# Performance work log

Hardware: AMD Instinct MI355X
Metric: run time of the kernel (lower is better)

Reference implementation:

```python
import jax, jax.numpy as jnp
import numpy as np

L, B, S, D, H, V = 6, 4, 1024, 1024, 16, 32000
HD = D // H          # head_size = 64
F = 4 * D            # ffn hidden
EPS = 1e-5           # nn.LayerNorm default


def setup_inputs() -> dict:
    key = jax.random.key(0)
    ks = jax.random.split(key, 12)
    s = 0.02
    p = {
        "tokens": jax.random.randint(ks[0], (B, S), 0, V, dtype=jnp.int32),
        "tok_emb": s * jax.random.normal(ks[1], (V, D), jnp.float32),
        "pos_emb": s * jax.random.normal(ks[2], (S, D), jnp.float32),
        # stacked per-layer params (leading dim L)
        "Wq": s * jax.random.normal(ks[3], (L, D, D), jnp.float32),
        "Wk": s * jax.random.normal(ks[4], (L, D, D), jnp.float32),
        "Wv": s * jax.random.normal(ks[5], (L, D, D), jnp.float32),
        "Wp": s * jax.random.normal(ks[6], (L, D, D), jnp.float32),
        "ln1_s": jnp.ones((L, D), jnp.float32),
        "ln1_b": jnp.zeros((L, D), jnp.float32),
        "W1": s * jax.random.normal(ks[7], (L, D, F), jnp.float32),
        "b1": jnp.zeros((L, F), jnp.float32),
        "W2": s * jax.random.normal(ks[8], (L, F, D), jnp.float32),
        "b2": jnp.zeros((L, D), jnp.float32),
        "ln2_s": jnp.ones((L, D), jnp.float32),
        "ln2_b": jnp.zeros((L, D), jnp.float32),
        "lnf_s": jnp.ones((D,), jnp.float32),
        "lnf_b": jnp.zeros((D,), jnp.float32),
        "Wh": s * jax.random.normal(ks[9], (D, V), jnp.float32),
        "bh": jnp.zeros((V,), jnp.float32),
    }
    return p


def _ln(x, scale, bias):
    m = x.mean(-1, keepdims=True)
    v = ((x - m) ** 2).mean(-1, keepdims=True)
    return (x - m) * jax.lax.rsqrt(v + EPS) * scale + bias


def reference(tokens, tok_emb, pos_emb, Wq, Wk, Wv, Wp, ln1_s, ln1_b,
              W1, b1, W2, b2, ln2_s, ln2_b, lnf_s, lnf_b, Wh, bh):
    x = tok_emb[tokens] + pos_emb[None, :, :]            # [B,S,D]
    mask = jnp.tril(jnp.ones((S, S), dtype=bool))
    inv_sqrt_hd = HD ** -0.5

    def layer(x, p):
        wq, wk, wv, wp, l1s, l1b, w1, b1_, w2, b2_, l2s, l2b = p
        q = jnp.einsum('bsd,dhk->bhsk', x, wq.reshape(D, H, HD))
        k = jnp.einsum('bsd,dhk->bhsk', x, wk.reshape(D, H, HD))
        v = jnp.einsum('bsd,dhk->bhsk', x, wv.reshape(D, H, HD))
        scores = jnp.einsum('bhsk,bhtk->bhst', q, k)     # [B,H,S,S]
        # original: masked_fill(-inf) THEN * head_size**-0.5 (same math: -inf stays -inf)
        scores = jnp.where(mask, scores * inv_sqrt_hd, -jnp.inf)
        attn = jax.nn.softmax(scores, axis=-1)
        o = jnp.einsum('bhst,bhtk->bhsk', attn, v)
        o = o.transpose(0, 2, 1, 3).reshape(B, S, D) @ wp
        a = x + _ln(o, l1s, l1b)                          # residual + ln1 (as in source)
        f = jax.nn.relu(a @ w1 + b1_) @ w2 + b2_
        return x + _ln(f, l2s, l2b), None                 # residual from block INPUT (as in source)

    x, _ = jax.lax.scan(layer, x,
                        (Wq, Wk, Wv, Wp, ln1_s, ln1_b, W1, b1, W2, b2, ln2_s, ln2_b))
    return _ln(x, lnf_s, lnf_b) @ Wh + bh                 # [B,S,V]
```

## Files before the change

### kernel.cpp

```cpp
#include <hip/hip_runtime.h>

#define DEV __device__ __forceinline__

typedef __attribute__((ext_vector_type(4))) float f32x4;
typedef __attribute__((ext_vector_type(8))) short short8_t;

constexpr int LNUM = 6;
constexpr int BB = 4;
constexpr int SS = 1024;
constexpr int DD = 1024;
constexpr int HH = 16;
constexpr int HDD = 64;
constexpr int FF = 4096;
constexpr int VV = 32000;
constexpr int MROWS = BB * SS;

DEV short f2bf(float f) {
  union { float f; unsigned u; } x; x.f = f;
  unsigned r = x.u + 0x7fffu + ((x.u >> 16) & 1u);
  return (short)(r >> 16);
}

#define BAR() do { __builtin_amdgcn_sched_barrier(0); \
  __builtin_amdgcn_s_barrier(); \
  __builtin_amdgcn_sched_barrier(0); } while (0)

__global__ __launch_bounds__(256) void k_embed(
    const int* __restrict__ tok, const float* __restrict__ te,
    const float* __restrict__ pe, float* __restrict__ xf,
    short* __restrict__ xb) {
  int i = blockIdx.x * 256 + threadIdx.x;
  int bs = i >> 8, d4 = i & 255;
  int t = tok[bs];
  float4 a = ((const float4*)(te + (size_t)t * DD))[d4];
  float4 b = ((const float4*)(pe + (size_t)(bs & (SS - 1)) * DD))[d4];
  float4 r; r.x = a.x + b.x; r.y = a.y + b.y; r.z = a.z + b.z; r.w = a.w + b.w;
  ((float4*)xf)[i] = r;
  short4 o; o.x = f2bf(r.x); o.y = f2bf(r.y); o.z = f2bf(r.z); o.w = f2bf(r.w);
  ((short4*)xb)[i] = o;
}

__global__ __launch_bounds__(256) void k_tcvt(
    const float* __restrict__ in, short* __restrict__ out, int K, int N,
    long long ostride) {
  __shared__ float tile[32][33];
  const float* ip = in + (size_t)blockIdx.z * K * N;
  short* op = out + (size_t)blockIdx.z * ostride;
  int bn = blockIdx.x * 32, bk = blockIdx.y * 32;
  int tx = threadIdx.x, ty = threadIdx.y;
  #pragma unroll
  for (int r = 0; r < 32; r += 8)
    tile[ty + r][tx] = ip[(size_t)(bk + ty + r) * N + bn + tx];
  __syncthreads();
  #pragma unroll
  for (int r = 0; r < 32; r += 8)
    op[(size_t)(bn + ty + r) * K + bk + tx] = f2bf(tile[tx][ty + r]);
}

DEV void gload16(const short* g, short* l) {
  __builtin_amdgcn_global_load_lds(
      (const __attribute__((address_space(1))) void*)g,
      (__attribute__((address_space(3))) void*)l, 16, 0, 0);
}

template<int MODE>
__global__ __launch_bounds__(512, 2) void k_gemm256(
    const short* __restrict__ A, const short* __restrict__ Bt,
    const float* __restrict__ bias, void* __restrict__ Cp,
    int M, int N, int K, int lda, int ldb) {
  extern __shared__ short lds[];
  const int tid = threadIdx.x;
  const int nbx = gridDim.x;
  const int nwg = nbx << 4;
  const int hid = blockIdx.y * nbx + blockIdx.x;
  const int cpx = nwg >> 3;
  const int lid = (hid & 7) * cpx + (hid >> 3);
  const int bx = lid >> 4, by = lid & 15;
  const int n0 = bx * 256, m0 = by * 256;

  const int lane = tid & 63;
  const int wid = tid >> 6;
  const int wm = wid >> 2, wn = wid & 3;
  const int l16 = lane & 15, kg = lane >> 4;
  const int xorv = (l16 & 7) << 4;
  const int cs[2] = { ((kg << 4) ^ xorv) >> 1,
                      ((64 | (kg << 4)) ^ xorv) >> 1 };
  const int rr = tid >> 3;
  const int sce = ((((tid & 7) << 4) ^ ((rr & 7) << 4)) >> 1);
  const int ldst = (tid & ~63) * 8;

  const int NT = K >> 6;

  auto stageA = [&](int t2, int c2) {
    const int k0 = t2 << 6;
    const int base = c2 * 32768;
    #pragma unroll
    for (int h = 0; h < 2; h++)
      #pragma unroll
      for (int li = 0; li < 2; li++)
        gload16(A + (size_t)(m0 + h * 128 + li * 64 + rr) * lda + k0 + sce,
                &lds[base + h * 8192 + li * 4096 + ldst]);
  };
  auto stageB = [&](int t2, int c2) {
    const int k0 = t2 << 6;
    const int base = c2 * 32768 + 16384;
    #pragma unroll
    for (int h = 0; h < 2; h++)
      #pragma unroll
      for (int li = 0; li < 2; li++)
        gload16(Bt + (size_t)(n0 + h * 128 + li * 64 + rr) * ldb + k0 + sce,
                &lds[base + h * 8192 + li * 4096 + ldst]);
  };

  f32x4 acc[8][4];
  #pragma unroll
  for (int mi = 0; mi < 8; mi++)
    #pragma unroll
    for (int ni = 0; ni < 4; ni++)
      #pragma unroll
      for (int j = 0; j < 4; j++) acc[mi][ni][j] = 0.f;

  stageA(0, 0); stageB(0, 0);
  stageA(1, 1); stageB(1, 1);
  asm volatile("s_waitcnt vmcnt(8)" ::: "memory");
  BAR();

  for (int t = 0; t < NT; t++) {
    const int c = t & 1;
    const int ao = c * 32768 + wm * 8192;
    const int bo = c * 32768 + 16384 + (wn >> 1) * 8192 + (wn & 1) * 4096;
    short8_t a[4][2], b0[2][2], b1[2][2];

    #pragma unroll
    for (int mi = 0; mi < 4; mi++)
      #pragma unroll
      for (int kk = 0; kk < 2; kk++)
        a[mi][kk] = *(const short8_t*)&lds[ao + (mi * 16 + l16) * 64 + cs[kk]];
    #pragma unroll
    for (int ni = 0; ni < 2; ni++)
      #pragma unroll
      for (int kk = 0; kk < 2; kk++)
        b0[ni][kk] = *(const short8_t*)&lds[bo + (ni * 16 + l16) * 64 + cs[kk]];
    BAR();
    __builtin_amdgcn_s_setprio(1);
    #pragma unroll
    for (int mi = 0; mi < 4; mi++)
      #pragma unroll
      for (int ni = 0; ni < 2; ni++)
        #pragma unroll
        for (int kk = 0; kk < 2; kk++)
          acc[mi][ni] = __builtin_amdgcn_mfma_f32_16x16x32_bf16(
              a[mi][kk], b0[ni][kk], acc[mi][ni], 0, 0, 0);
    __builtin_amdgcn_s_setprio(0);
    BAR();

    #pragma unroll
    for (int ni = 0; ni < 2; ni++)
      #pragma unroll
      for (int kk = 0; kk < 2; kk++)
        b1[ni][kk] = *(const short8_t*)&lds[bo + ((ni + 2) * 16 + l16) * 64 + cs[kk]];
    BAR();
    __builtin_amdgcn_s_setprio(1);
    #pragma unroll
    for (int mi = 0; mi < 4; mi++)
      #pragma unroll
      for (int ni = 0; ni < 2; ni++)
        #pragma unroll
        for (int kk = 0; kk < 2; kk++)
          acc[mi][ni + 2] = __builtin_amdgcn_mfma_f32_16x16x32_bf16(
              a[mi][kk], b1[ni][kk], acc[mi][ni + 2], 0, 0, 0);
    __builtin_amdgcn_s_setprio(0);
    BAR();

    #pragma unroll
    for (int mi = 0; mi < 4; mi++)
      #pragma unroll
      for (int kk = 0; kk < 2; kk++)
        a[mi][kk] = *(const short8_t*)&lds[ao + ((mi + 4) * 16 + l16) * 64 + cs[kk]];
    if (t + 2 < NT) stageB(t + 2, c);
    BAR();
    __builtin_amdgcn_s_setprio(1);
    #pragma unroll
    for (int mi = 0; mi < 4; mi++)
      #pragma unroll
      for (int ni = 0; ni < 2; ni++)
        #pragma unroll
        for (int kk = 0; kk < 2; kk++)
          acc[mi + 4][ni + 2] = __builtin_amdgcn_mfma_f32_16x16x32_bf16(
              a[mi][kk], b1[ni][kk], acc[mi + 4][ni + 2], 0, 0, 0);
    __builtin_amdgcn_s_setprio(0);
    BAR();

    if (t + 2 < NT) stageA(t + 2, c);
    BAR();
    __builtin_amdgcn_s_setprio(1);
    #pragma unroll
    for (int mi = 0; mi < 4; mi++)
      #pragma unroll
      for (int ni = 0; ni < 2; ni++)
        #pragma unroll
        for (int kk = 0; kk < 2; kk++)
          acc[mi + 4][ni] = __builtin_amdgcn_mfma_f32_16x16x32_bf16(
              a[mi][kk], b0[ni][kk], acc[mi + 4][ni], 0, 0, 0);
    __builtin_amdgcn_s_setprio(0);
    if (t + 2 < NT) asm volatile("s_waitcnt vmcnt(8)" ::: "memory");
    else            asm volatile("s_waitcnt vmcnt(0)" ::: "memory");
    BAR();
  }

  #pragma unroll
  for (int mi = 0; mi < 8; mi++) {
    #pragma unroll
    for (int ni = 0; ni < 4; ni++) {
      #pragma unroll
      for (int j = 0; j < 4; j++) {
        const int r = m0 + wm * 128 + mi * 16 + kg * 4 + j;
        const int c = n0 + wn * 64 + ni * 16 + l16;
        const float v = acc[mi][ni][j];
        if (MODE == 5) {
          ((float*)Cp)[(size_t)r * N + c] = v;
        } else if (MODE == 6) {
          ((short*)Cp)[(size_t)r * N + c] = f2bf(fmaxf(v + bias[c], 0.f));
        } else if (MODE == 7) {
          ((float*)Cp)[(size_t)r * N + c] = v + bias[c];
        } else if (MODE == 8) {
          int kind = c >> 10, cc = c & 1023;
          int b = r >> 10, s = r & 1023, h = cc >> 6, hd = cc & 63;
          size_t off;
          if (kind < 2)
            off = (size_t)kind * MROWS * DD +
                  (((size_t)(b * HH + h) << 10) + s) * HDD + hd;
          else
            off = (size_t)2 * MROWS * DD +
                  (((size_t)(b * HH + h) * HDD + hd) << 10) + s;
          ((short*)Cp)[off] = f2bf(v);
        }
      }
    }
  }
}

#define RDSWZ(arr, r, cb) \
  (*(const short8_t*)&arr[((r) << 6) + ((((cb) ^ (((r) & 7) << 4))) >> 1)])
#define RDSWZ7(arr, r, cb) \
  (*(const short8_t*)&arr[((r) << 7) + ((((cb) ^ (((r) & 7) << 4))) >> 1)])

__global__ __launch_bounds__(256, 2) void k_attn(
    const short* __restrict__ Qg, const short* __restrict__ Kgl,
    const short* __restrict__ Vt, short* __restrict__ Og) {
  extern __shared__ short sm[];
  short* lQ = sm;
  short* lK = sm + 8192;
  short* lV = sm + 16384;
  short* lP = sm + 24576;
  const int tid = threadIdx.x;
  const int qb = blockIdx.x, z = blockIdx.y;
  const int q0 = qb << 7;
  const short* Qp = Qg + ((size_t)z << 16);
  const short* Kp = Kgl + ((size_t)z << 16);
  const short* Vp = Vt + ((size_t)z << 16);
  const int bidx = z >> 4, h = z & 15;
  const int lane = tid & 63, w = tid >> 6;
  const int l16 = lane & 15, kg = lane >> 4;
  const int sr = tid >> 3;
  const int scb = ((((tid & 7) << 4) ^ ((sr & 7) << 4)) >> 1);
  const int vr = tid >> 4;
  const int vcb = ((((tid & 15) << 4) ^ ((vr & 7) << 4)) >> 1);
  const int ldst = (tid & ~63) << 3;

  #pragma unroll
  for (int i = 0; i < 4; i++)
    gload16(Qp + ((size_t)(q0 + i * 32 + sr) << 6) + scb, &lQ[i * 2048 + ldst]);

  f32x4 acc_o[2][4];
  float m_r[2][4], l_r[2][4];
  #pragma unroll
  for (int mi = 0; mi < 2; mi++)
    #pragma unroll
    for (int j = 0; j < 4; j++) {
      m_r[mi][j] = -3e38f; l_r[mi][j] = 0.f;
      #pragma unroll
      for (int n2 = 0; n2 < 4; n2++) acc_o[mi][n2][j] = 0.f;
    }

  const int nkt = qb + 1;
  for (int kt = 0; kt < nkt; kt++) {
    const int k0 = kt << 7;
    #pragma unroll
    for (int i = 0; i < 4; i++)
      gload16(Kp + ((size_t)(k0 + i * 32 + sr) << 6) + scb, &lK[i * 2048 + ldst]);
    #pragma unroll
    for (int i = 0; i < 4; i++)
      gload16(Vp + ((size_t)(i * 16 + vr) << 10) + k0 + vcb, &lV[i * 2048 + ldst]);
    __syncthreads();

    f32x4 s[2][8];
    #pragma unroll
    for (int mi = 0; mi < 2; mi++)
      #pragma unroll
      for (int nf = 0; nf < 8; nf++)
        #pragma unroll
        for (int j = 0; j < 4; j++) s[mi][nf][j] = 0.f;
    #pragma unroll
    for (int kk = 0; kk < 2; kk++) {
      short8_t aq[2];
      #pragma unroll
      for (int mi = 0; mi < 2; mi++)
        aq[mi] = RDSWZ(lQ, w * 32 + mi * 16 + l16, kk * 64 + kg * 16);
      #pragma unroll
      for (int nf = 0; nf < 8; nf++) {
        short8_t bk = RDSWZ(lK, nf * 16 + l16, kk * 64 + kg * 16);
        #pragma unroll
        for (int mi = 0; mi < 2; mi++)
          s[mi][nf] = __builtin_amdgcn_mfma_f32_16x16x32_bf16(
              aq[mi], bk, s[mi][nf], 0, 0, 0);
      }
    }

    const bool diag = (kt == qb);
    #pragma unroll
    for (int mi = 0; mi < 2; mi++) {
      #pragma unroll
      for (int j = 0; j < 4; j++) {
        const int ql = w * 32 + mi * 16 + kg * 4 + j;
        const int q = q0 + ql;
        float sv[8]; float tm = -3e38f;
        #pragma unroll
        for (int nf = 0; nf < 8; nf++) {
          int kv = k0 + nf * 16 + l16;
          sv[nf] = (!diag || kv <= q) ? s[mi][nf][j] * 0.125f : -3e38f;
          tm = fmaxf(tm, sv[nf]);
        }
        #pragma unroll
        for (int o = 1; o < 16; o <<= 1) tm = fmaxf(tm, __shfl_xor(tm, o));
        const float mn = fmaxf(m_r[mi][j], tm);
        const float scale = __expf(m_r[mi][j] - mn);
        float e[8]; float ts = 0.f;
        #pragma unroll
        for (int nf = 0; nf < 8; nf++) { e[nf] = __expf(sv[nf] - mn); ts += e[nf]; }
        #pragma unroll
        for (int o = 1; o < 16; o <<= 1) ts += __shfl_xor(ts, o);
        l_r[mi][j] = l_r[mi][j] * scale + ts;
        m_r[mi][j] = mn;
        #pragma unroll
        for (int n2 = 0; n2 < 4; n2++) acc_o[mi][n2][j] *= scale;
        #pragma unroll
        for (int nf = 0; nf < 8; nf++)
          lP[(ql << 7) + ((nf * 16 + l16) ^ ((ql & 7) << 3))] = f2bf(e[nf]);
      }
    }

    #pragma unroll
    for (int kc = 0; kc < 4; kc++) {
      short8_t pa[2];
      #pragma unroll
      for (int mi = 0; mi < 2; mi++) {
        const int pr = w * 32 + mi * 16 + l16;
        pa[mi] = *(const short8_t*)
            &lP[(pr << 7) + ((kc * 32 + kg * 8) ^ ((pr & 7) << 3))];
      }
      #pragma unroll
      for (int n2 = 0; n2 < 4; n2++) {
        short8_t vb = RDSWZ7(lV, n2 * 16 + l16, kc * 64 + kg * 16);
        #pragma unroll
        for (int mi = 0; mi < 2; mi++)
          acc_o[mi][n2] = __builtin_amdgcn_mfma_f32_16x16x32_bf16(
              pa[mi], vb, acc_o[mi][n2], 0, 0, 0);
      }
    }
    __syncthreads();
  }

  #pragma unroll
  for (int mi = 0; mi < 2; mi++) {
    #pragma unroll
    for (int j = 0; j < 4; j++) {
      const int q = q0 + w * 32 + mi * 16 + kg * 4 + j;
      const float inv = 1.f / l_r[mi][j];
      #pragma unroll
      for (int n2 = 0; n2 < 4; n2++) {
        const int col = h * HDD + n2 * 16 + l16;
        Og[(((size_t)bidx << 10) + q) * DD + col] = f2bf(acc_o[mi][n2][j] * inv);
      }
    }
  }
}

template<int ADD_RES, int WRITE_F32>
__global__ __launch_bounds__(256) void k_ln(
    const float* __restrict__ src, const float* __restrict__ res,
    const float* __restrict__ g, const float* __restrict__ b,
    float* __restrict__ of, short* __restrict__ ob) {
  const int row = blockIdx.x;
  const int tid = threadIdx.x;
  float4 v = ((const float4*)(src + ((size_t)row << 10)))[tid];
  float s1 = v.x + v.y + v.z + v.w;
  float s2 = v.x * v.x + v.y * v.y + v.z * v.z + v.w * v.w;
  #pragma unroll
  for (int o = 32; o; o >>= 1) { s1 += __shfl_xor(s1, o); s2 += __shfl_xor(s2, o); }
  __shared__ float sh1[4], sh2[4];
  if ((tid & 63) == 0) { sh1[tid >> 6] = s1; sh2[tid >> 6] = s2; }
  __syncthreads();
  s1 = sh1[0] + sh1[1] + sh1[2] + sh1[3];
  s2 = sh2[0] + sh2[1] + sh2[2] + sh2[3];
  const float mean = s1 * (1.f / 1024.f);
  const float var  = s2 * (1.f / 1024.f) - mean * mean;
  const float rs = rsqrtf(var + 1e-5f);
  float4 gg = ((const float4*)g)[tid];
  float4 bb = ((const float4*)b)[tid];
  float4 o4;
  o4.x = (v.x - mean) * rs * gg.x + bb.x;
  o4.y = (v.y - mean) * rs * gg.y + bb.y;
  o4.z = (v.z - mean) * rs * gg.z + bb.z;
  o4.w = (v.w - mean) * rs * gg.w + bb.w;
  if (ADD_RES) {
    float4 rr = ((const float4*)(res + ((size_t)row << 10)))[tid];
    o4.x += rr.x; o4.y += rr.y; o4.z += rr.z; o4.w += rr.w;
  }
  if (WRITE_F32) ((float4*)(of + ((size_t)row << 10)))[tid] = o4;
  short4 s4; s4.x = f2bf(o4.x); s4.y = f2bf(o4.y);
  s4.z = f2bf(o4.z); s4.w = f2bf(o4.w);
  ((short4*)ob)[((size_t)row << 8) + tid] = s4;
}

extern "C" void kernel_launch(void* const* d_in, const int* in_sizes, int n_in,
                              void* d_out, int out_size, void* d_ws, size_t ws_size,
                              hipStream_t stream) {
  (void)in_sizes; (void)n_in; (void)out_size; (void)ws_size;
  const int*   tokens  = (const int*)d_in[0];
  const float* tok_emb = (const float*)d_in[1];
  const float* pos_emb = (const float*)d_in[2];
  const float* Wq = (const float*)d_in[3];
  const float* Wk = (const float*)d_in[4];
  const float* Wv = (const float*)d_in[5];
  const float* Wp = (const float*)d_in[6];
  const float* ln1s = (const float*)d_in[7];
  const float* ln1b = (const float*)d_in[8];
  const float* W1 = (const float*)d_in[9];
  const float* b1 = (const float*)d_in[10];
  const float* W2 = (const float*)d_in[11];
  const float* b2 = (const float*)d_in[12];
  const float* ln2s = (const float*)d_in[13];
  const float* ln2b = (const float*)d_in[14];
  const float* lnfs = (const float*)d_in[15];
  const float* lnfb = (const float*)d_in[16];
  const float* Wh = (const float*)d_in[17];
  const float* bh = (const float*)d_in[18];
  float* out = (float*)d_out;

  hipFuncSetAttribute((const void*)k_gemm256<5>,
      hipFuncAttributeMaxDynamicSharedMemorySize, 131072);
  hipFuncSetAttribute((const void*)k_gemm256<6>,
      hipFuncAttributeMaxDynamicSharedMemorySize, 131072);
  hipFuncSetAttribute((const void*)k_gemm256<7>,
      hipFuncAttributeMaxDynamicSharedMemorySize, 131072);
  hipFuncSetAttribute((const void*)k_gemm256<8>,
      hipFuncAttributeMaxDynamicSharedMemorySize, 131072);
  hipFuncSetAttribute((const void*)k_attn,
      hipFuncAttributeMaxDynamicSharedMemorySize, 81920);

  char* p = (char*)d_ws;
  auto alloc = [&](size_t elems, size_t esz) -> char* {
    char* r = p; p += (elems * esz + 255) & ~(size_t)255; return r;
  };
  short* WqkvT = (short*)alloc((size_t)LNUM * 3 * DD * DD, 2);
  short* WpT = (short*)alloc((size_t)LNUM * DD * DD, 2);
  short* W1T = (short*)alloc((size_t)LNUM * DD * FF, 2);
  short* W2T = (short*)alloc((size_t)LNUM * DD * FF, 2);
  short* WhT = (short*)alloc((size_t)DD * VV, 2);
  float* xf   = (float*)alloc((size_t)MROWS * DD, 4);
  float* ff   = (float*)alloc((size_t)MROWS * DD, 4);
  short* xb   = (short*)alloc((size_t)MROWS * DD, 2);
  short* ab   = (short*)alloc((size_t)MROWS * DD, 2);
  short* qkvb = (short*)alloc((size_t)3 * MROWS * DD, 2);
  short* obuf = (short*)alloc((size_t)MROWS * DD, 2);
  short* hb   = (short*)alloc((size_t)MROWS * FF, 2);
  short* xfb  = (short*)alloc((size_t)MROWS * DD, 2);
  short* qb   = qkvb;
  short* kb   = qkvb + (size_t)MROWS * DD;
  short* vtb  = qkvb + (size_t)2 * MROWS * DD;

  dim3 blk(256);
  dim3 t8(32, 8);
  const long long DD2 = (long long)DD * DD;
  k_tcvt<<<dim3(DD / 32, DD / 32, LNUM), t8, 0, stream>>>(Wq, WqkvT,          DD, DD, 3 * DD2);
  k_tcvt<<<dim3(DD / 32, DD / 32, LNUM), t8, 0, stream>>>(Wk, WqkvT + DD2,    DD, DD, 3 * DD2);
  k_tcvt<<<dim3(DD / 32, DD / 32, LNUM), t8, 0, stream>>>(Wv, WqkvT + 2*DD2,  DD, DD, 3 * DD2);
  k_tcvt<<<dim3(DD / 32, DD / 32, LNUM), t8, 0, stream>>>(Wp, WpT, DD, DD, DD2);
  k_tcvt<<<dim3(FF / 32, DD / 32, LNUM), t8, 0, stream>>>(W1, W1T, DD, FF, (long long)DD * FF);
  k_tcvt<<<dim3(DD / 32, FF / 32, LNUM), t8, 0, stream>>>(W2, W2T, FF, DD, (long long)DD * FF);
  k_tcvt<<<dim3(VV / 32, DD / 32, 1),   t8, 0, stream>>>(Wh, WhT, DD, VV, 0);

  k_embed<<<(MROWS * DD / 4) / 256, blk, 0, stream>>>(tokens, tok_emb, pos_emb, xf, xb);

  for (int l = 0; l < LNUM; l++) {
    const short* wqkv = WqkvT + (size_t)l * 3 * DD * DD;
    const short* wp = WpT + (size_t)l * DD * DD;
    const short* w1 = W1T + (size_t)l * DD * FF;
    const short* w2 = W2T + (size_t)l * DD * FF;

    k_gemm256<8><<<dim3(12, 16), 512, 131072, stream>>>(xb, wqkv, nullptr, qkvb,
        MROWS, 3 * DD, DD, DD, DD);
    k_attn<<<dim3(8, BB * HH), blk, 81920, stream>>>(qb, kb, vtb, obuf);
    k_gemm256<5><<<dim3(4, 16), 512, 131072, stream>>>(obuf, wp, nullptr, ff,
        MROWS, DD, DD, DD, DD);
    k_ln<1, 0><<<MROWS, blk, 0, stream>>>(ff, xf, ln1s + (size_t)l * DD,
        ln1b + (size_t)l * DD, nullptr, ab);
    k_gemm256<6><<<dim3(16, 16), 512, 131072, stream>>>(ab, w1, b1 + (size_t)l * FF, hb,
        MROWS, FF, DD, DD, DD);
    k_gemm256<7><<<dim3(4, 16), 512, 131072, stream>>>(hb, w2, b2 + (size_t)l * DD, ff,
        MROWS, DD, FF, FF, FF);
    k_ln<1, 1><<<MROWS, blk, 0, stream>>>(ff, xf, ln2s + (size_t)l * DD,
        ln2b + (size_t)l * DD, xf, xb);
  }

  k_ln<0, 0><<<MROWS, blk, 0, stream>>>(xf, nullptr, lnfs, lnfb, nullptr, xfb);
  k_gemm256<7><<<dim3(VV / 256, 16), 512, 131072, stream>>>(xfb, WhT, bh, out,
      MROWS, VV, DD, DD, DD);
}
```

Before: 2.443 ms.

## Use 128x128 GEMM for N=1024 projections, interleave head-GEMM stores, reverse attention order

The Wp and W2 projections (N=1024) move from the 256x256 tile kernel, which launched only 64 blocks, to a new simple 128x128-tile kernel launching 256 blocks. This is meant to fill more compute units on those narrow GEMMs. The simple kernel has no double buffering, so it may stall on global loads. The final vocab GEMM gets a mode that stores each quarter of the accumulator right after its last MFMA group, so output writes overlap the remaining compute. Attention blocks for the second half of batch-heads run query blocks in reverse order to balance the causal workload across the launch.

```diff
diff --git a/kernel.cpp b/kernel.cpp
--- a/kernel.cpp
+++ b/kernel.cpp
@@ -120,6 +120,19 @@
       #pragma unroll
       for (int j = 0; j < 4; j++) acc[mi][ni][j] = 0.f;
 
+  auto storeQ = [&](int mlo, int nlo) {
+    #pragma unroll
+    for (int mi = 0; mi < 4; mi++)
+      #pragma unroll
+      for (int ni = 0; ni < 2; ni++)
+        #pragma unroll
+        for (int j = 0; j < 4; j++) {
+          const int r = m0 + wm * 128 + (mlo + mi) * 16 + kg * 4 + j;
+          const int c = n0 + wn * 64 + (nlo + ni) * 16 + l16;
+          ((float*)Cp)[(size_t)r * N + c] = acc[mlo + mi][nlo + ni][j] + bias[c];
+        }
+  };
+
   stageA(0, 0); stageB(0, 0);
   stageA(1, 1); stageB(1, 1);
   asm volatile("s_waitcnt vmcnt(8)" ::: "memory");
@@ -152,6 +165,7 @@
           acc[mi][ni] = __builtin_amdgcn_mfma_f32_16x16x32_bf16(
               a[mi][kk], b0[ni][kk], acc[mi][ni], 0, 0, 0);
     __builtin_amdgcn_s_setprio(0);
+    if (MODE == 9 && t == NT - 1) storeQ(0, 0);
     BAR();
 
     #pragma unroll
@@ -170,6 +184,7 @@
           acc[mi][ni + 2] = __builtin_amdgcn_mfma_f32_16x16x32_bf16(
               a[mi][kk], b1[ni][kk], acc[mi][ni + 2], 0, 0, 0);
     __builtin_amdgcn_s_setprio(0);
+    if (MODE == 9 && t == NT - 1) storeQ(0, 2);
     BAR();
 
     #pragma unroll
@@ -189,6 +204,7 @@
           acc[mi + 4][ni + 2] = __builtin_amdgcn_mfma_f32_16x16x32_bf16(
               a[mi][kk], b1[ni][kk], acc[mi + 4][ni + 2], 0, 0, 0);
     __builtin_amdgcn_s_setprio(0);
+    if (MODE == 9 && t == NT - 1) storeQ(4, 2);
     BAR();
 
     if (t + 2 < NT) stageA(t + 2, c);
@@ -208,6 +224,10 @@
     BAR();
   }
 
+  if (MODE == 9) {
+    storeQ(4, 0);
+    return;
+  }
   #pragma unroll
   for (int mi = 0; mi < 8; mi++) {
     #pragma unroll
@@ -217,12 +237,8 @@
         const int r = m0 + wm * 128 + mi * 16 + kg * 4 + j;
         const int c = n0 + wn * 64 + ni * 16 + l16;
         const float v = acc[mi][ni][j];
-        if (MODE == 5) {
-          ((float*)Cp)[(size_t)r * N + c] = v;
-        } else if (MODE == 6) {
+        if (MODE == 6) {
           ((short*)Cp)[(size_t)r * N + c] = f2bf(fmaxf(v + bias[c], 0.f));
-        } else if (MODE == 7) {
-          ((float*)Cp)[(size_t)r * N + c] = v + bias[c];
         } else if (MODE == 8) {
           int kind = c >> 10, cc = c & 1023;
           int b = r >> 10, s = r & 1023, h = cc >> 6, hd = cc & 63;
@@ -240,6 +256,75 @@
   }
 }
 
+template<int MODE>
+__global__ __launch_bounds__(256) void k_gemm(
+    const short* __restrict__ A, const short* __restrict__ Bt,
+    const float* __restrict__ bias, void* __restrict__ Cp,
+    int M, int N, int K, int lda, int ldb) {
+  __shared__ short lA[4096];
+  __shared__ short lB[4096];
+  const int tid = threadIdx.x;
+  const int n0 = blockIdx.x * 128, m0 = blockIdx.y * 128;
+
+  const int lane = tid & 63;
+  const int wm = (tid >> 6) >> 1, wn = (tid >> 6) & 1;
+  const int l16 = lane & 15, kg = lane >> 4;
+  const int srow = tid >> 2, scol = (tid & 3) * 8;
+  const int lbase = (tid & ~63) * 8;
+
+  f32x4 acc[4][4];
+  #pragma unroll
+  for (int a = 0; a < 4; a++)
+    #pragma unroll
+    for (int b = 0; b < 4; b++)
+      #pragma unroll
+      for (int j = 0; j < 4; j++) acc[a][b][j] = 0.f;
+
+  for (int k0 = 0; k0 < K; k0 += 32) {
+    #pragma unroll
+    for (int i = 0; i < 2; i++)
+      gload16(A + (size_t)(m0 + i * 64 + srow) * lda + (k0 + scol),
+              &lA[i * 2048 + lbase]);
+    #pragma unroll
+    for (int i = 0; i < 2; i++)
+      gload16(Bt + (size_t)(n0 + i * 64 + srow) * ldb + (k0 + scol),
+              &lB[i * 2048 + lbase]);
+    __syncthreads();
+    short8_t af[4], bf[4];
+    #pragma unroll
+    for (int mi = 0; mi < 4; mi++)
+      af[mi] = *(const short8_t*)&lA[(wm * 64 + mi * 16 + l16) * 32 + kg * 8];
+    #pragma unroll
+    for (int ni = 0; ni < 4; ni++)
+      bf[ni] = *(const short8_t*)&lB[(wn * 64 + ni * 16 + l16) * 32 + kg * 8];
+    #pragma unroll
+    for (int mi = 0; mi < 4; mi++)
+      #pragma unroll
+      for (int ni = 0; ni < 4; ni++)
+        acc[mi][ni] = __builtin_amdgcn_mfma_f32_16x16x32_bf16(
+            af[mi], bf[ni], acc[mi][ni], 0, 0, 0);
+    __syncthreads();
+  }
+
+  #pragma unroll
+  for (int mi = 0; mi < 4; mi++) {
+    #pragma unroll
+    for (int ni = 0; ni < 4; ni++) {
+      #pragma unroll
+      for (int j = 0; j < 4; j++) {
+        const int r = m0 + wm * 64 + mi * 16 + kg * 4 + j;
+        const int c = n0 + wn * 64 + ni * 16 + l16;
+        const float v = acc[mi][ni][j];
+        if (MODE == 5) {
+          ((float*)Cp)[(size_t)r * N + c] = v;
+        } else if (MODE == 7) {
+          ((float*)Cp)[(size_t)r * N + c] = v + bias[c];
+        }
+      }
+    }
+  }
+}
+
 #define RDSWZ(arr, r, cb) \
   (*(const short8_t*)&arr[((r) << 6) + ((((cb) ^ (((r) & 7) << 4))) >> 1)])
 #define RDSWZ7(arr, r, cb) \
@@ -254,7 +339,8 @@
   short* lV = sm + 16384;
   short* lP = sm + 24576;
   const int tid = threadIdx.x;
-  const int qb = blockIdx.x, z = blockIdx.y;
+  const int z = blockIdx.y;
+  const int qb = (z < 32) ? blockIdx.x : 7 - blockIdx.x;
   const int q0 = qb << 7;
   const short* Qp = Qg + ((size_t)z << 16);
   const short* Kp = Kgl + ((size_t)z << 16);
@@ -448,13 +534,11 @@
   const float* bh = (const float*)d_in[18];
   float* out = (float*)d_out;
 
-  hipFuncSetAttribute((const void*)k_gemm256<5>,
-      hipFuncAttributeMaxDynamicSharedMemorySize, 131072);
   hipFuncSetAttribute((const void*)k_gemm256<6>,
       hipFuncAttributeMaxDynamicSharedMemorySize, 131072);
-  hipFuncSetAttribute((const void*)k_gemm256<7>,
+  hipFuncSetAttribute((const void*)k_gemm256<8>,
       hipFuncAttributeMaxDynamicSharedMemorySize, 131072);
-  hipFuncSetAttribute((const void*)k_gemm256<8>,
+  hipFuncSetAttribute((const void*)k_gemm256<9>,
       hipFuncAttributeMaxDynamicSharedMemorySize, 131072);
   hipFuncSetAttribute((const void*)k_attn,
       hipFuncAttributeMaxDynamicSharedMemorySize, 81920);
@@ -502,19 +586,19 @@
     k_gemm256<8><<<dim3(12, 16), 512, 131072, stream>>>(xb, wqkv, nullptr, qkvb,
         MROWS, 3 * DD, DD, DD, DD);
     k_attn<<<dim3(8, BB * HH), blk, 81920, stream>>>(qb, kb, vtb, obuf);
-    k_gemm256<5><<<dim3(4, 16), 512, 131072, stream>>>(obuf, wp, nullptr, ff,
+    k_gemm<5><<<dim3(8, 32), blk, 0, stream>>>(obuf, wp, nullptr, ff,
         MROWS, DD, DD, DD, DD);
     k_ln<1, 0><<<MROWS, blk, 0, stream>>>(ff, xf, ln1s + (size_t)l * DD,
         ln1b + (size_t)l * DD, nullptr, ab);
     k_gemm256<6><<<dim3(16, 16), 512, 131072, stream>>>(ab, w1, b1 + (size_t)l * FF, hb,
         MROWS, FF, DD, DD, DD);
-    k_gemm256<7><<<dim3(4, 16), 512, 131072, stream>>>(hb, w2, b2 + (size_t)l * DD, ff,
+    k_gemm<7><<<dim3(8, 32), blk, 0, stream>>>(hb, w2, b2 + (size_t)l * DD, ff,
         MROWS, DD, FF, FF, FF);
     k_ln<1, 1><<<MROWS, blk, 0, stream>>>(ff, xf, ln2s + (size_t)l * DD,
         ln2b + (size_t)l * DD, xf, xb);
   }
 
   k_ln<0, 0><<<MROWS, blk, 0, stream>>>(xf, nullptr, lnfs, lnfb, nullptr, xfb);
-  k_gemm256<7><<<dim3(VV / 256, 16), 512, 131072, stream>>>(xfb, WhT, bh, out,
+  k_gemm256<9><<<dim3(VV / 256, 16), 512, 131072, stream>>>(xfb, WhT, bh, out,
       MROWS, VV, DD, DD, DD);
 }
```

Result: no change. 2.418 ms (-1.0%).
